# Kernel tuning notes

Measured on AMD Instinct MI355X. Metric: run time of the kernel, lower is better.

## Reference

```python
import jax, jax.numpy as jnp
import numpy as np

EPS = 1e-5
NUM_HEADS = 32

def layer_norm(x, g, b):
    m = jnp.mean(x, axis=-1, keepdims=True)
    v = jnp.mean((x - m) ** 2, axis=-1, keepdims=True)
    return (x - m) * jax.lax.rsqrt(v + EPS) * g + b

def positional_encoding(S, E):
    pos = jnp.arange(S, dtype=jnp.float32)[:, None]
    div = jnp.exp(jnp.arange(0, E, 2, dtype=jnp.float32) * (-jnp.log(10000.0) / E))
    ang = pos * div  # [S, E/2]
    pe = jnp.zeros((S, E), jnp.float32)
    pe = pe.at[:, 0::2].set(jnp.sin(ang)).at[:, 1::2].set(jnp.cos(ang))
    return pe

def quantum_attention(x, phi_l):
    # QLayer circuit: RX(x_j + phi_j) per wire, CNOT ring, measure Z.
    # Heisenberg picture: <Z_i> = prod_{j<=i} cos(a_j) for i>=1,
    #                     <Z_0> = prod_{j>=1} cos(a_j), a_j = x_j + phi_j.
    B, S, E = x.shape
    dk = E // NUM_HEADS  # = 8 wires
    c = jnp.cos(x.reshape(B, S, NUM_HEADS, dk) + phi_l)  # per-wire <Z> factor
    pref = jnp.cumprod(c, axis=-1)                       # prod_{j<=i}
    out0 = jnp.prod(c[..., 1:], axis=-1)                 # wire 0
    q = jnp.concatenate([out0[..., None], pref[..., 1:]], axis=-1)
    q = q.reshape(B, S, E)
    scores = jax.nn.softmax(
        jnp.einsum('bse,bte->bst', q, q) / jnp.sqrt(jnp.float32(dk)), axis=-1)
    return jnp.einsum('bst,bte->bse', scores, q)

def quantum_ffn(x, theta_l, W1_l, b1_l, W2_l, b2_l):
    # QLayer: RX(x_i) then RY(theta_i) on |0>, product state => <Z_i>=cos(x_i)cos(theta_i)
    nq = theta_l.shape[0]  # 8; encoder only reads first nq features
    qm = jnp.cos(x[..., :nq]) * jnp.cos(theta_l)
    h = jax.nn.relu(qm @ W1_l + b1_l)
    return h @ W2_l + b2_l

def setup_inputs() -> dict:
    key = jax.random.key(0)
    ks = jax.random.split(key, 10)
    V, E, L, FF, NQ, NC = 32000, 256, 4, 1024, 8, 10
    B, S = 8, 2048
    return {
        'tokens': jax.random.randint(ks[0], (B, S), 0, V, dtype=jnp.int64)
            if jax.config.jax_enable_x64 else jax.random.randint(ks[0], (B, S), 0, V, dtype=jnp.int32),
        'emb': jax.random.normal(ks[1], (V, E), jnp.float32),
        'phi': jax.random.normal(ks[2], (L, NQ), jnp.float32),
        'theta': jax.random.normal(ks[3], (L, NQ), jnp.float32),
        'W1': jax.random.normal(ks[4], (L, NQ, FF), jnp.float32) * 0.1,
        'b1': jax.random.normal(ks[5], (L, FF), jnp.float32) * 0.1,
        'W2': jax.random.normal(ks[6], (L, FF, E), jnp.float32) * 0.05,
        'b2': jax.random.normal(ks[7], (L, E), jnp.float32) * 0.05,
        'g1': jnp.ones((L, E), jnp.float32),
        'beta1': jnp.zeros((L, E), jnp.float32),
        'g2': jnp.ones((L, E), jnp.float32),
        'beta2': jnp.zeros((L, E), jnp.float32),
        'Wc': jax.random.normal(ks[8], (E, NC), jnp.float32) * 0.05,
        'bc': jax.random.normal(ks[9], (NC,), jnp.float32) * 0.05,
    }

def reference(tokens, emb, phi, theta, W1, b1, W2, b2, g1, beta1, g2, beta2, Wc, bc):
    B, S = tokens.shape
    E = emb.shape[1]
    x = emb[tokens] + positional_encoding(S, E)
    for l in range(phi.shape[0]):  # fixed num_blocks loop
        a = quantum_attention(x, phi[l])
        x = layer_norm(x + a, g1[l], beta1[l])
        f = quantum_ffn(x, theta[l], W1[l], b1[l], W2[l], b2[l])
        x = layer_norm(x + f, g2[l], beta2[l])
    return jnp.mean(x, axis=1) @ Wc + bc
```

## Files before the change

kernel.cpp:

```cpp
#include <hip/hip_runtime.h>
#include <hip/hip_bf16.h>

#define B_ 8
#define S_ 2048
#define E_ 256
#define FF_ 1024
#define NQ_ 8
#define NC_ 10
#define BS_ (B_*S_)
#define NSPLIT 2
#define KVBLK 32

typedef __bf16 bf16x8 __attribute__((ext_vector_type(8)));
typedef float f32x4 __attribute__((ext_vector_type(4)));

#define MFMA16(a,b,c) __builtin_amdgcn_mfma_f32_16x16x32_bf16(a,b,c,0,0,0)

__global__ __launch_bounds__(256) void k_embed(const int* __restrict__ tokens,
                                               const float* __restrict__ emb,
                                               float* __restrict__ x) {
    int row = blockIdx.x;
    int e = threadIdx.x;
    int s = row & (S_ - 1);
    int tok = tokens[row];
    int i2 = e & ~1;
    float d = __expf((float)i2 * (-9.210340371976184f / 256.0f));
    float ang = (float)s * d;
    float pe = (e & 1) ? __cosf(ang) : __sinf(ang);
    x[(size_t)row * E_ + e] = emb[(size_t)tok * E_ + e] + pe;
}

__global__ __launch_bounds__(256) void k_qt(const float* __restrict__ x,
                                            const float* __restrict__ phi_l,
                                            __hip_bfloat16* __restrict__ qbf,
                                            __hip_bfloat16* __restrict__ qT) {
    __shared__ __align__(16) __bf16 tile[64][76];
    int t0 = blockIdx.x * 64, e0 = blockIdx.y * 64, b = blockIdx.z;
    int tid = threadIdx.x;
    float ph[8];
#pragma unroll
    for (int j = 0; j < 8; j++) ph[j] = phi_l[j];
#pragma unroll
    for (int k = 0; k < 2; k++) {
        int idx = k * 256 + tid;
        int r = idx >> 3, hh = idx & 7;
        const float* xp = x + ((size_t)b * S_ + t0 + r) * E_ + e0 + hh * 8;
        f32x4 x0 = *(const f32x4*)xp;
        f32x4 x1 = *(const f32x4*)(xp + 4);
        float c[8];
#pragma unroll
        for (int j = 0; j < 4; j++) {
            c[j]     = __cosf(x0[j] + ph[j]);
            c[4 + j] = __cosf(x1[j] + ph[4 + j]);
        }
        float q[8];
        float run = c[0];
#pragma unroll
        for (int i = 1; i < 8; i++) { run *= c[i]; q[i] = run; }
        float o0 = c[1];
#pragma unroll
        for (int i = 2; i < 8; i++) o0 *= c[i];
        q[0] = o0;
        bf16x8 v;
#pragma unroll
        for (int j = 0; j < 8; j++) v[j] = (__bf16)q[j];
        *(bf16x8*)(qbf + ((size_t)b * S_ + t0 + r) * E_ + e0 + hh * 8) = v;
        *(bf16x8*)&tile[r][hh * 8] = v;
    }
    __syncthreads();
#pragma unroll
    for (int k = 0; k < 2; k++) {
        int idx = k * 256 + tid;
        int el = idx >> 3, tc = idx & 7;
        bf16x8 v;
#pragma unroll
        for (int j = 0; j < 8; j++) v[j] = tile[tc * 8 + j][el];
        *(bf16x8*)(qT + ((size_t)b * E_ + e0 + el) * S_ + t0 + tc * 8) = v;
    }
}

__global__ __launch_bounds__(256, 2) void k_attn(const __hip_bfloat16* __restrict__ qbf,
                                                 const __hip_bfloat16* __restrict__ qT,
                                                 float* __restrict__ pacc,
                                                 float* __restrict__ pl) {
    __shared__ __align__(16) __bf16 ktile[KVBLK * 256];
    __shared__ __align__(16) __bf16 vtile[2][256 * KVBLK];
    __shared__ __align__(16) __bf16 plds[2][32][36];
    __shared__ float redl[2][32][2];
    const float SCALE = 0.3535533905932738f;
    int bid  = blockIdx.x;
    int b    = bid & 7;
    int qt   = (bid >> 3) & 31;
    int z    = bid >> 8;
    int tid  = threadIdx.x;
    int wv   = tid >> 6;
    int lane = tid & 63;
    int r16  = lane & 15;
    int kg   = lane >> 4;
    int rg   = wv >> 1, eh = wv & 1;
    int qrow0 = qt * 64 + rg * 32;
    int ebase = eh * 128;

    bf16x8 aq[2][8];
#pragma unroll
    for (int qs = 0; qs < 2; qs++)
#pragma unroll
        for (int kk = 0; kk < 8; kk++)
            aq[qs][kk] = *(const bf16x8*)(qbf + ((size_t)b * S_ + qrow0 + qs * 16 + r16) * E_ + kk * 32 + kg * 8);

    f32x4 acc0[8], acc1[8];
#pragma unroll
    for (int cf = 0; cf < 8; cf++) { acc0[cf] = (f32x4){0.f,0.f,0.f,0.f}; acc1[cf] = (f32x4){0.f,0.f,0.f,0.f}; }
    float lrow0[4] = {0.f,0.f,0.f,0.f}, lrow1[4] = {0.f,0.f,0.f,0.f};

    constexpr int SPAN = S_ / NSPLIT;
    constexpr int NT = SPAN / KVBLK;
    int k0 = z * SPAN;

    auto issue_k = [&](int kb) {
#pragma unroll
        for (int c = 0; c < 4; c++) {
            int seg = wv * 4 + c;
            int r = seg * 2 + (lane >> 5);
            int ch = lane & 31;
            const __hip_bfloat16* src = qbf + ((size_t)b * S_ + kb + r) * E_ + ((ch ^ (r & 7)) * 8);
            __builtin_amdgcn_global_load_lds((const __attribute__((address_space(1))) void*)src,
                                             (__attribute__((address_space(3))) void*)(ktile + seg * 512),
                                             16, 0, 0);
        }
    };
    auto issue_v = [&](int kb, int buf) {
#pragma unroll
        for (int c = 0; c < 4; c++) {
            int seg = wv * 4 + c;
            int e = seg * 16 + (lane >> 2);
            int ch = lane & 3;
            const __hip_bfloat16* src = qT + ((size_t)b * E_ + e) * S_ + kb + ((ch ^ ((e >> 1) & 3)) * 8);
            __builtin_amdgcn_global_load_lds((const __attribute__((address_space(1))) void*)src,
                                             (__attribute__((address_space(3))) void*)(&vtile[buf][seg * 512]),
                                             16, 0, 0);
        }
    };

    issue_k(k0);
    issue_v(k0, 0);
    asm volatile("s_waitcnt vmcnt(0)" ::: "memory");
    __syncthreads();

    for (int kt = 0; kt < NT; kt++) {
        int vcur = kt & 1;
        f32x4 s0 = (f32x4){0.f,0.f,0.f,0.f}, s1 = (f32x4){0.f,0.f,0.f,0.f};
#pragma unroll
        for (int kk = 0; kk < 8; kk++) {
            bf16x8 bk = *(const bf16x8*)&ktile[(eh * 16 + r16) * 256 + (((kk * 4 + kg) ^ (r16 & 7)) * 8)];
            s0 = MFMA16(aq[0][kk], bk, s0);
            s1 = MFMA16(aq[1][kk], bk, s1);
        }
#pragma unroll
        for (int i = 0; i < 4; i++) {
            float p0 = __expf(fmaf(s0[i], SCALE, -44.0f));
            float p1 = __expf(fmaf(s1[i], SCALE, -44.0f));
            plds[rg][kg * 4 + i][eh * 16 + r16]      = (__bf16)p0;
            plds[rg][16 + kg * 4 + i][eh * 16 + r16] = (__bf16)p1;
            lrow0[i] += p0;
            lrow1[i] += p1;
        }
        __syncthreads();
        bool more = (kt + 1 < NT);
        if (more) {
            int kn = k0 + (kt + 1) * KVBLK;
            issue_k(kn);
            issue_v(kn, vcur ^ 1);
        }
        bf16x8 pa0 = *(const bf16x8*)&plds[rg][r16][kg * 8];
        bf16x8 pa1 = *(const bf16x8*)&plds[rg][16 + r16][kg * 8];
#pragma unroll
        for (int cf = 0; cf < 8; cf++) {
            int vrow = ebase + cf * 16 + r16;
            bf16x8 bv = *(const bf16x8*)&vtile[vcur][vrow * KVBLK + ((kg ^ ((vrow >> 1) & 3)) * 8)];
            acc0[cf] = MFMA16(pa0, bv, acc0[cf]);
            acc1[cf] = MFMA16(pa1, bv, acc1[cf]);
        }
        if (more) {
            asm volatile("s_waitcnt vmcnt(0)" ::: "memory");
            __syncthreads();
        }
    }

#pragma unroll
    for (int i = 0; i < 4; i++) {
#pragma unroll
        for (int m = 1; m <= 8; m <<= 1) {
            lrow0[i] += __shfl_xor(lrow0[i], m);
            lrow1[i] += __shfl_xor(lrow1[i], m);
        }
    }
    if (r16 == 0) {
#pragma unroll
        for (int i = 0; i < 4; i++) {
            redl[rg][kg * 4 + i][eh]      = lrow0[i];
            redl[rg][16 + kg * 4 + i][eh] = lrow1[i];
        }
    }
    __syncthreads();
    size_t prow0 = (size_t)z * BS_ + (size_t)b * S_ + qrow0;
    if (eh == 0 && r16 == 0) {
#pragma unroll
        for (int i = 0; i < 4; i++) {
            int q = kg * 4 + i;
            pl[prow0 + q]      = redl[rg][q][0] + redl[rg][q][1];
            pl[prow0 + 16 + q] = redl[rg][16 + q][0] + redl[rg][16 + q][1];
        }
    }
#pragma unroll
    for (int i = 0; i < 4; i++) {
#pragma unroll
        for (int cf = 0; cf < 8; cf++) {
            pacc[(prow0 + kg * 4 + i) * E_ + ebase + cf * 16 + r16]      = acc0[cf][i];
            pacc[(prow0 + 16 + kg * 4 + i) * E_ + ebase + cf * 16 + r16] = acc1[cf][i];
        }
    }
}

__global__ __launch_bounds__(256) void k_aln(const float* __restrict__ pacc,
                                             const float* __restrict__ pl,
                                             float* __restrict__ x,
                                             const float* __restrict__ g,
                                             const float* __restrict__ bb) {
    int wv = threadIdx.x >> 6, lane = threadIdx.x & 63;
    size_t row = (size_t)blockIdx.x * 4 + wv;
    float inv = 1.0f / (pl[row] + pl[BS_ + row]);
    f32x4 a0 = ((const f32x4*)(pacc + row * E_))[lane];
    f32x4 a1 = ((const f32x4*)(pacc + (size_t)BS_ * E_ + row * E_))[lane];
    f32x4 xv = ((const f32x4*)(x + row * E_))[lane];
    f32x4 v;
    float s = 0.f, sq = 0.f;
#pragma unroll
    for (int j = 0; j < 4; j++) {
        v[j] = xv[j] + (a0[j] + a1[j]) * inv;
        s += v[j]; sq += v[j] * v[j];
    }
#pragma unroll
    for (int m = 1; m <= 32; m <<= 1) { s += __shfl_xor(s, m); sq += __shfl_xor(sq, m); }
    float mean = s * (1.f / E_);
    float var = sq * (1.f / E_) - mean * mean;
    float rstd = rsqrtf(var + 1e-5f);
    f32x4 gv = ((const f32x4*)g)[lane];
    f32x4 bv = ((const f32x4*)bb)[lane];
    f32x4 o;
#pragma unroll
    for (int j = 0; j < 4; j++) o[j] = (v[j] - mean) * rstd * gv[j] + bv[j];
    ((f32x4*)(x + row * E_))[lane] = o;
}

__global__ __launch_bounds__(256) void k_w2t(const float* __restrict__ W2l,
                                             __hip_bfloat16* __restrict__ w2t) {
    __shared__ __align__(16) __bf16 tile[64][72];
    int k0 = blockIdx.x * 64, e0 = blockIdx.y * 64;
    int tid = threadIdx.x;
#pragma unroll
    for (int half = 0; half < 2; half++) {
        int r  = half * 32 + (tid >> 3);
        int c8 = (tid & 7) * 8;
        f32x4 v0 = *(const f32x4*)(W2l + (size_t)(k0 + r) * E_ + e0 + c8);
        f32x4 v1 = *(const f32x4*)(W2l + (size_t)(k0 + r) * E_ + e0 + c8 + 4);
#pragma unroll
        for (int j = 0; j < 4; j++) { tile[r][c8 + j] = (__bf16)v0[j]; tile[r][c8 + 4 + j] = (__bf16)v1[j]; }
    }
    __syncthreads();
#pragma unroll
    for (int half = 0; half < 2; half++) {
        int e  = half * 32 + (tid >> 3);
        int k8 = (tid & 7) * 8;
        bf16x8 v;
#pragma unroll
        for (int j = 0; j < 8; j++) v[j] = tile[k8 + j][e];
        *(bf16x8*)(w2t + (size_t)(e0 + e) * FF_ + k0 + k8) = v;
    }
}

__global__ __launch_bounds__(256) void k_ffn(const float* __restrict__ x,
                                             const float* __restrict__ theta_l,
                                             const float* __restrict__ W1l,
                                             const float* __restrict__ b1l,
                                             const __hip_bfloat16* __restrict__ w2t,
                                             const float* __restrict__ b2l,
                                             const float* __restrict__ g,
                                             const float* __restrict__ bb) {
    __shared__ __align__(16) __bf16 Bld[2][256 * 64];
    __shared__ __align__(16) __bf16 Ald[2][32 * 64];
    __shared__ float qmld[32][9];
    __shared__ float reds[32][4][2];
    int tid = threadIdx.x;
    int wv = tid >> 6, lane = tid & 63;
    int r16 = lane & 15, kg = lane >> 4;
    int rbase = blockIdx.x * 32;
    int ebQ = wv * 64;
    const int NT = FF_ / 64;

    {
        int r = tid >> 3, i = tid & 7;
        qmld[r][i] = __cosf(x[(size_t)(rbase + r) * E_ + i]) * __cosf(theta_l[i]);
    }

    f32x4 w[18];

    auto issue_B = [&](int kt, int buf) {
#pragma unroll
        for (int s = 0; s < 8; s++) {
            int seg = wv * 8 + s;
            int e = seg * 8 + (lane >> 3);
            int c = lane & 7;
            const __hip_bfloat16* src = w2t + (size_t)e * FF_ + kt * 64 + ((c ^ (e & 7)) * 8);
            __builtin_amdgcn_global_load_lds((const __attribute__((address_space(1))) void*)src,
                                             (__attribute__((address_space(3))) void*)(&Bld[buf][seg * 512]),
                                             16, 0, 0);
        }
    };
    auto load_W1 = [&](int kt) {
        int c = tid & 7;
        int k = kt * 64 + c * 8;
#pragma unroll
        for (int i = 0; i < 8; i++) {
            w[2 * i]     = *(const f32x4*)(W1l + (size_t)i * FF_ + k);
            w[2 * i + 1] = *(const f32x4*)(W1l + (size_t)i * FF_ + k + 4);
        }
        w[16] = *(const f32x4*)(b1l + k);
        w[17] = *(const f32x4*)(b1l + k + 4);
    };
    auto math_h = [&](int buf) {
        int r = tid >> 3, c = tid & 7;
        f32x4 h0 = w[16], h1 = w[17];
#pragma unroll
        for (int i = 0; i < 8; i++) {
            float qv = qmld[r][i];
#pragma unroll
            for (int j = 0; j < 4; j++) {
                h0[j] = fmaf(qv, w[2 * i][j], h0[j]);
                h1[j] = fmaf(qv, w[2 * i + 1][j], h1[j]);
            }
        }
        bf16x8 hv;
#pragma unroll
        for (int j = 0; j < 4; j++) {
            hv[j]     = (__bf16)fmaxf(h0[j], 0.f);
            hv[4 + j] = (__bf16)fmaxf(h1[j], 0.f);
        }
        *(bf16x8*)&Ald[buf][r * 64 + ((c ^ (r & 7)) * 8)] = hv;
    };

    issue_B(0, 0);
    load_W1(0);
    __syncthreads();
    math_h(0);
    __syncthreads();

    f32x4 acc[2][4];
#pragma unroll
    for (int qs = 0; qs < 2; qs++)
#pragma unroll
        for (int cf = 0; cf < 4; cf++) acc[qs][cf] = (f32x4){0.f, 0.f, 0.f, 0.f};

    for (int kt = 0; kt < NT; kt++) {
        int cur = kt & 1;
        bool more = (kt + 1 < NT);
        if (more) {
            issue_B(kt + 1, cur ^ 1);
            load_W1(kt + 1);
        }
        bf16x8 aq[2][2];
#pragma unroll
        for (int qs = 0; qs < 2; qs++)
#pragma unroll
            for (int kk = 0; kk < 2; kk++)
                aq[qs][kk] = *(const bf16x8*)&Ald[cur][(qs * 16 + r16) * 64 + (((kk * 4 + kg) ^ (r16 & 7)) * 8)];
#pragma unroll
        for (int cf = 0; cf < 4; cf++) {
            int e = ebQ + cf * 16 + r16;
#pragma unroll
            for (int kk = 0; kk < 2; kk++) {
                bf16x8 bv = *(const bf16x8*)&Bld[cur][e * 64 + (((kk * 4 + kg) ^ (e & 7)) * 8)];
                acc[0][cf] = MFMA16(aq[0][kk], bv, acc[0][cf]);
                acc[1][cf] = MFMA16(aq[1][kk], bv, acc[1][cf]);
            }
        }
        if (more) {
            math_h(cur ^ 1);
            __syncthreads();
        }
    }

    float sA[2][4] = {{0.f,0.f,0.f,0.f},{0.f,0.f,0.f,0.f}};
    float sQ[2][4] = {{0.f,0.f,0.f,0.f},{0.f,0.f,0.f,0.f}};
#pragma unroll
    for (int qs = 0; qs < 2; qs++)
#pragma unroll
        for (int cf = 0; cf < 4; cf++) {
            int e = ebQ + cf * 16 + r16;
            float b2v = b2l[e];
#pragma unroll
            for (int i = 0; i < 4; i++) {
                size_t orow = (size_t)rbase + qs * 16 + kg * 4 + i;
                float t = acc[qs][cf][i] + b2v + x[orow * E_ + e];
                acc[qs][cf][i] = t;
                sA[qs][i] += t; sQ[qs][i] += t * t;
            }
        }
#pragma unroll
    for (int qs = 0; qs < 2; qs++)
#pragma unroll
        for (int i = 0; i < 4; i++) {
#pragma unroll
            for (int m = 1; m <= 8; m <<= 1) {
                sA[qs][i] += __shfl_xor(sA[qs][i], m);
                sQ[qs][i] += __shfl_xor(sQ[qs][i], m);
            }
        }
    if (r16 == 0) {
#pragma unroll
        for (int qs = 0; qs < 2; qs++)
#pragma unroll
            for (int i = 0; i < 4; i++) {
                int row = qs * 16 + kg * 4 + i;
                reds[row][wv][0] = sA[qs][i];
                reds[row][wv][1] = sQ[qs][i];
            }
    }
    __syncthreads();
    float mean[2][4], rstd[2][4];
#pragma unroll
    for (int qs = 0; qs < 2; qs++)
#pragma unroll
        for (int i = 0; i < 4; i++) {
            int row = qs * 16 + kg * 4 + i;
            float S = reds[row][0][0] + reds[row][1][0] + reds[row][2][0] + reds[row][3][0];
            float Q = reds[row][0][1] + reds[row][1][1] + reds[row][2][1] + reds[row][3][1];
            mean[qs][i] = S * (1.f / E_);
            float var = Q * (1.f / E_) - mean[qs][i] * mean[qs][i];
            rstd[qs][i] = rsqrtf(var + 1e-5f);
        }
    float* xo = (float*)x;
#pragma unroll
    for (int qs = 0; qs < 2; qs++)
#pragma unroll
        for (int cf = 0; cf < 4; cf++) {
            int e = ebQ + cf * 16 + r16;
            float gv = g[e], bv = bb[e];
#pragma unroll
            for (int i = 0; i < 4; i++) {
                size_t orow = (size_t)rbase + qs * 16 + kg * 4 + i;
                xo[orow * E_ + e] = (acc[qs][cf][i] - mean[qs][i]) * rstd[qs][i] * gv + bv;
            }
        }
}

__global__ __launch_bounds__(256) void k_mean(const float* __restrict__ x, float* __restrict__ psum) {
    int c = blockIdx.x, b = blockIdx.y, e = threadIdx.x;
    float s = 0.f;
    size_t base = ((size_t)b * S_ + c * 128) * E_ + e;
    for (int r = 0; r < 128; r++) s += x[base + (size_t)r * E_];
    psum[(c * 8 + b) * E_ + e] = s;
}

__global__ __launch_bounds__(256) void k_mean2(const float* __restrict__ psum, float* __restrict__ xmean) {
    int idx = blockIdx.x * 256 + threadIdx.x;
    int b = idx >> 8, e = idx & 255;
    float s = 0.f;
    for (int c = 0; c < 16; c++) s += psum[(c * 8 + b) * E_ + e];
    xmean[idx] = s * (1.f / S_);
}

__global__ __launch_bounds__(128) void k_cls(const float* __restrict__ xmean,
                                             const float* __restrict__ Wc,
                                             const float* __restrict__ bc,
                                             float* __restrict__ outp) {
    int t = threadIdx.x;
    if (t >= B_ * NC_) return;
    int b = t / NC_, c = t % NC_;
    float s = bc[c];
    for (int e = 0; e < E_; e++) s += xmean[b * E_ + e] * Wc[e * NC_ + c];
    outp[t] = s;
}

extern "C" void kernel_launch(void* const* d_in, const int* in_sizes, int n_in,
                              void* d_out, int out_size, void* d_ws, size_t ws_size,
                              hipStream_t stream) {
    (void)in_sizes; (void)n_in; (void)out_size; (void)ws_size;
    const int*   tokens = (const int*)d_in[0];
    const float* emb    = (const float*)d_in[1];
    const float* phi    = (const float*)d_in[2];
    const float* theta  = (const float*)d_in[3];
    const float* W1     = (const float*)d_in[4];
    const float* b1     = (const float*)d_in[5];
    const float* W2     = (const float*)d_in[6];
    const float* b2     = (const float*)d_in[7];
    const float* g1     = (const float*)d_in[8];
    const float* beta1  = (const float*)d_in[9];
    const float* g2     = (const float*)d_in[10];
    const float* beta2  = (const float*)d_in[11];
    const float* Wc     = (const float*)d_in[12];
    const float* bc     = (const float*)d_in[13];
    float* outp = (float*)d_out;

    float* xbuf = (float*)d_ws;
    __hip_bfloat16* qbf = (__hip_bfloat16*)(xbuf + (size_t)BS_ * E_);
    __hip_bfloat16* qT  = qbf + (size_t)BS_ * E_;
    __hip_bfloat16* w2t = qT + (size_t)BS_ * E_;
    float* psum  = (float*)(w2t + (size_t)E_ * FF_);
    float* xmean = psum + 16 * 8 * E_;
    float* pl    = xmean + B_ * E_;
    float* pacc  = pl + (size_t)NSPLIT * BS_;

    k_embed<<<BS_, 256, 0, stream>>>(tokens, emb, xbuf);

    for (int l = 0; l < 4; l++) {
        k_qt<<<dim3(S_ / 64, E_ / 64, B_), 256, 0, stream>>>(xbuf, phi + l * NQ_, qbf, qT);
        k_attn<<<(S_ / 64) * B_ * NSPLIT, 256, 0, stream>>>(qbf, qT, pacc, pl);
        k_aln<<<BS_ / 4, 256, 0, stream>>>(pacc, pl, xbuf, g1 + l * E_, beta1 + l * E_);
        k_w2t<<<dim3(FF_ / 64, E_ / 64), 256, 0, stream>>>(W2 + (size_t)l * FF_ * E_, w2t);
        k_ffn<<<BS_ / 32, 256, 0, stream>>>(xbuf, theta + l * NQ_,
                                            W1 + (size_t)l * NQ_ * FF_, b1 + (size_t)l * FF_,
                                            w2t, b2 + (size_t)l * E_,
                                            g2 + l * E_, beta2 + l * E_);
    }

    k_mean<<<dim3(16, B_), 256, 0, stream>>>(xbuf, psum);
    k_mean2<<<8, 256, 0, stream>>>(psum, xmean);
    k_cls<<<1, 128, 0, stream>>>(xmean, Wc, bc, outp);
}
```

Baseline: 450.1 us.

## Load attention V fragments directly into registers and hoist W2 transposes

The attention kernel stops staging V tiles through double-buffered LDS with async global-to-LDS copies. Each lane now loads its V fragments straight from global memory into registers at the top of each KV step, which frees LDS and may raise occupancy, but it gives up the prefetch overlap and issues less-coalesced 16-byte loads. Separately, the four per-layer W2 transposes are launched once up front into a larger workspace, so they no longer sit between the layer kernels. The workspace layout grows to hold all four transposed W2 matrices.

Result: slower. 588.0 us (+30.6%).

```diff
diff --git a/kernel.cpp b/kernel.cpp
--- a/kernel.cpp
+++ b/kernel.cpp
@@ -84,7 +84,6 @@
                                                  float* __restrict__ pacc,
                                                  float* __restrict__ pl) {
     __shared__ __align__(16) __bf16 ktile[KVBLK * 256];
-    __shared__ __align__(16) __bf16 vtile[2][256 * KVBLK];
     __shared__ __align__(16) __bf16 plds[2][32][36];
     __shared__ float redl[2][32][2];
     const float SCALE = 0.3535533905932738f;
@@ -129,26 +128,23 @@
                                              16, 0, 0);
         }
     };
-    auto issue_v = [&](int kb, int buf) {
-#pragma unroll
-        for (int c = 0; c < 4; c++) {
-            int seg = wv * 4 + c;
-            int e = seg * 16 + (lane >> 2);
-            int ch = lane & 3;
-            const __hip_bfloat16* src = qT + ((size_t)b * E_ + e) * S_ + kb + ((ch ^ ((e >> 1) & 3)) * 8);
-            __builtin_amdgcn_global_load_lds((const __attribute__((address_space(1))) void*)src,
-                                             (__attribute__((address_space(3))) void*)(&vtile[buf][seg * 512]),
-                                             16, 0, 0);
+
+    bf16x8 bv[8];
+    auto issue_bv = [&](int kb) {
+#pragma unroll
+        for (int cf = 0; cf < 8; cf++) {
+            int vrow = ebase + cf * 16 + r16;
+            bv[cf] = *(const bf16x8*)(qT + ((size_t)b * E_ + vrow) * S_ + kb + kg * 8);
         }
     };
 
     issue_k(k0);
-    issue_v(k0, 0);
     asm volatile("s_waitcnt vmcnt(0)" ::: "memory");
     __syncthreads();
 
     for (int kt = 0; kt < NT; kt++) {
-        int vcur = kt & 1;
+        int kbase = k0 + kt * KVBLK;
+        issue_bv(kbase);
         f32x4 s0 = (f32x4){0.f,0.f,0.f,0.f}, s1 = (f32x4){0.f,0.f,0.f,0.f};
 #pragma unroll
         for (int kk = 0; kk < 8; kk++) {
@@ -167,19 +163,13 @@
         }
         __syncthreads();
         bool more = (kt + 1 < NT);
-        if (more) {
-            int kn = k0 + (kt + 1) * KVBLK;
-            issue_k(kn);
-            issue_v(kn, vcur ^ 1);
-        }
+        if (more) issue_k(kbase + KVBLK);
         bf16x8 pa0 = *(const bf16x8*)&plds[rg][r16][kg * 8];
         bf16x8 pa1 = *(const bf16x8*)&plds[rg][16 + r16][kg * 8];
 #pragma unroll
         for (int cf = 0; cf < 8; cf++) {
-            int vrow = ebase + cf * 16 + r16;
-            bf16x8 bv = *(const bf16x8*)&vtile[vcur][vrow * KVBLK + ((kg ^ ((vrow >> 1) & 3)) * 8)];
-            acc0[cf] = MFMA16(pa0, bv, acc0[cf]);
-            acc1[cf] = MFMA16(pa1, bv, acc1[cf]);
+            acc0[cf] = MFMA16(pa0, bv[cf], acc0[cf]);
+            acc1[cf] = MFMA16(pa1, bv[cf], acc1[cf]);
         }
         if (more) {
             asm volatile("s_waitcnt vmcnt(0)" ::: "memory");
@@ -506,21 +496,23 @@
     __hip_bfloat16* qbf = (__hip_bfloat16*)(xbuf + (size_t)BS_ * E_);
     __hip_bfloat16* qT  = qbf + (size_t)BS_ * E_;
     __hip_bfloat16* w2t = qT + (size_t)BS_ * E_;
-    float* psum  = (float*)(w2t + (size_t)E_ * FF_);
+    float* psum  = (float*)(w2t + (size_t)4 * E_ * FF_);
     float* xmean = psum + 16 * 8 * E_;
     float* pl    = xmean + B_ * E_;
     float* pacc  = pl + (size_t)NSPLIT * BS_;
 
     k_embed<<<BS_, 256, 0, stream>>>(tokens, emb, xbuf);
+    for (int l = 0; l < 4; l++)
+        k_w2t<<<dim3(FF_ / 64, E_ / 64), 256, 0, stream>>>(W2 + (size_t)l * FF_ * E_,
+                                                           w2t + (size_t)l * E_ * FF_);
 
     for (int l = 0; l < 4; l++) {
         k_qt<<<dim3(S_ / 64, E_ / 64, B_), 256, 0, stream>>>(xbuf, phi + l * NQ_, qbf, qT);
         k_attn<<<(S_ / 64) * B_ * NSPLIT, 256, 0, stream>>>(qbf, qT, pacc, pl);
         k_aln<<<BS_ / 4, 256, 0, stream>>>(pacc, pl, xbuf, g1 + l * E_, beta1 + l * E_);
-        k_w2t<<<dim3(FF_ / 64, E_ / 64), 256, 0, stream>>>(W2 + (size_t)l * FF_ * E_, w2t);
         k_ffn<<<BS_ / 32, 256, 0, stream>>>(xbuf, theta + l * NQ_,
                                             W1 + (size_t)l * NQ_ * FF_, b1 + (size_t)l * FF_,
-                                            w2t, b2 + (size_t)l * E_,
+                                            w2t + (size_t)l * E_ * FF_, b2 + (size_t)l * E_,
                                             g2 + l * E_, beta2 + l * E_);
     }
 
```
